# Optimization experiments

Measured on AMD Instinct MI355X. Metric: run time of the kernel, lower is better.

Reference implementation:

```python
import jax, jax.numpy as jnp
import numpy as np

DIM = 768
H = 12  # num_heads -> head width W = 64 (required by internal reshapes)


def setup_inputs() -> dict:
    key = jax.random.key(0)
    ks = jax.random.split(key, 16)
    B, S = 1, 128  # V = Q = A = 128 tokens
    d = {
        "v": jax.random.normal(ks[0], (B, S, DIM), jnp.float32),
        "q": jax.random.normal(ks[1], (B, S, DIM), jnp.float32),
        "a": jax.random.normal(ks[2], (B, S, DIM), jnp.float32),
        "v_mask": jnp.ones((B, S), jnp.bool_),  # unused by the module, kept for signature parity
        "q_mask": jnp.ones((B, S), jnp.bool_),
        "a_mask": jnp.ones((B, S), jnp.bool_),
    }
    scale = 0.02
    names = ["Wv", "Wq", "Wa", "Wvo", "Wqo", "Wao"]
    for i, n in enumerate(names):
        d[n] = jax.random.normal(ks[3 + i], (DIM, DIM), jnp.float32) * scale
        d["b" + n[1:].lower()] = jnp.zeros((DIM,), jnp.float32)
    return d


def _heads(x):
    # (B, S, D) -> (B, H, S, W)
    B, S, D = x.shape
    return x.reshape(B, S, H, D // H).transpose(0, 2, 1, 3)


def reference(v, q, a, v_mask, q_mask, a_mask,
              Wv, bv, Wq, bq, Wa, ba, Wvo, bvo, Wqo, bqo, Wao, bao):
    B, Sv, D = v.shape
    Sq, Sa = q.shape[1], a.shape[1]
    W = D // H
    nv, nq, na = Sv // 8, Sq // 8, Sa // 8

    # first projections (masks are unused in the original forward)
    vp = v @ Wv + bv
    qp = q @ Wq + bq
    ap = a @ Wa + ba
    # output projections are applied to the ALREADY-projected tensors (as in source)
    vo = vp @ Wvo + bvo
    qo = qp @ Wqo + bqo
    ao = ap @ Wao + bao

    vh, qh, ah = _heads(vp), _heads(qp), _heads(ap)          # (B,H,S,W)
    voh, qoh, aoh = _heads(vo), _heads(qo), _heads(ao)

    # trilinear scores: (B,H,V,Q,A)
    att = jnp.einsum('bhvw,bhqw,bhaw->bhvqa', vh, qh, ah) / jnp.sqrt(jnp.asarray(W, vh.dtype))
    K = nv * nq * na
    # faithful to source: view(-1, H, nv*nq*na) then softmax over last axis, view back
    att = jax.nn.softmax(att.reshape(-1, H, K), axis=-1)
    att = att.reshape(-1, H, nv, nq, na)  # dropout p=0 -> identity
    B2 = att.shape[0]

    # source uses att.size(2) (= nv) for ALL three reshapes (requires V=Q=A)
    vor = voh.reshape(B2, H, nv, -1)
    qor = qoh.reshape(B2, H, nv, -1)
    aor = aoh.reshape(B2, H, nv, -1)

    v_out = jnp.einsum('bhvqa,bhvw->bvhw', att, vor).reshape(-1, DIM)
    q_out = jnp.einsum('bhvqa,bhqw->bqhw', att, qor).reshape(-1, DIM)
    a_out = jnp.einsum('bhvqa,bhaw->bahw', att, aor).reshape(-1, DIM)
    return (v_out, q_out, a_out)
```

## Files before the change

kernel.cpp:

```cpp
#include <hip/hip_runtime.h>


#define DIM   768
#define SEQ   128
#define NH    12
#define HW    64
#define PROJ_ELEMS (SEQ * DIM)
#define WELEMS     (DIM * DIM)
#define QOUT_OFF   98304
#define AOUT_OFF   196608

typedef _Float16 f16x8 __attribute__((ext_vector_type(8)));
typedef float    f32x4 __attribute__((ext_vector_type(4)));

__device__ __forceinline__ float exp2_fast(float x) {
    float r;
    asm("v_exp_f32 %0, %1\n\ts_nop 1" : "=v"(r) : "v"(x));
    return r;
}
#define LOG2E_DIV8 0.18033688011112042f

__global__ __launch_bounds__(256) void prep_w_kernel(
    const float* __restrict__ W0, const float* __restrict__ W1, const float* __restrict__ W2,
    const float* __restrict__ W3, const float* __restrict__ W4, const float* __restrict__ W5,
    _Float16* __restrict__ Wt)
{
    const int z = blockIdx.z;
    const float* W = (z == 0) ? W0 : (z == 1) ? W1 : (z == 2) ? W2
                   : (z == 3) ? W3 : (z == 4) ? W4 : W5;
    _Float16* WtM = Wt + z * WELEMS;
    __shared__ _Float16 T[64][72];
    const int t  = threadIdx.x;
    const int k0 = blockIdx.x * 64;
    const int n0 = blockIdx.y * 64;
    const int c4 = (t & 15) * 4;
    #pragma unroll
    for (int p = 0; p < 4; ++p) {
        const int r = (t >> 4) + 16 * p;
        f32x4 wv = *(const f32x4*)&W[(k0 + r) * DIM + n0 + c4];
        T[c4 + 0][r] = (_Float16)wv[0];
        T[c4 + 1][r] = (_Float16)wv[1];
        T[c4 + 2][r] = (_Float16)wv[2];
        T[c4 + 3][r] = (_Float16)wv[3];
    }
    __syncthreads();
    const int c2 = (t & 7) * 8;
    #pragma unroll
    for (int p = 0; p < 2; ++p) {
        const int r = (t >> 3) + 32 * p;
        *(f16x8*)&WtM[(n0 + r) * DIM + k0 + c2] = *(const f16x8*)&T[r][c2];
    }
}

__global__ __launch_bounds__(64) void proj_kernel(
    const void* __restrict__ A0, const void* __restrict__ A1, const void* __restrict__ A2,
    const _Float16* __restrict__ T0, const _Float16* __restrict__ T1, const _Float16* __restrict__ T2,
    const float* __restrict__ b0, const float* __restrict__ b1, const float* __restrict__ b2,
    void* __restrict__ C0, void* __restrict__ C1, void* __restrict__ C2,
    int in_f32, int out_f16)
{
    const int mat = blockIdx.z;
    const void* __restrict__ A     = (mat == 0) ? A0 : (mat == 1) ? A1 : A2;
    const _Float16* __restrict__ T = (mat == 0) ? T0 : (mat == 1) ? T1 : T2;
    const float* __restrict__ bb   = (mat == 0) ? b0 : (mat == 1) ? b1 : b2;
    void* __restrict__ C           = (mat == 0) ? C0 : (mat == 1) ? C1 : C2;

    const int m0   = blockIdx.x * 16;
    const int n0   = blockIdx.y * 16;
    const int lane = threadIdx.x & 63;
    const int fm   = lane & 15;
    const int fk   = (lane >> 4) << 3;

    const _Float16* pb = T + (n0 + fm) * DIM + fk;
    f32x4 acc = (f32x4){0.f, 0.f, 0.f, 0.f};

    if (in_f32) {
        const float* pa = (const float*)A + (m0 + fm) * DIM + fk;
        #pragma unroll 4
        for (int s = 0; s < 24; ++s) {
            const f32x4 lo = *(const f32x4*)(pa + 32 * s);
            const f32x4 hi = *(const f32x4*)(pa + 32 * s + 4);
            f16x8 af;
            af[0] = (_Float16)lo[0]; af[1] = (_Float16)lo[1];
            af[2] = (_Float16)lo[2]; af[3] = (_Float16)lo[3];
            af[4] = (_Float16)hi[0]; af[5] = (_Float16)hi[1];
            af[6] = (_Float16)hi[2]; af[7] = (_Float16)hi[3];
            const f16x8 wf = *(const f16x8*)(pb + 32 * s);
            acc = __builtin_amdgcn_mfma_f32_16x16x32_f16(af, wf, acc, 0, 0, 0);
        }
    } else {
        const _Float16* pa = (const _Float16*)A + (m0 + fm) * DIM + fk;
        #pragma unroll 4
        for (int s = 0; s < 24; ++s) {
            const f16x8 af = *(const f16x8*)(pa + 32 * s);
            const f16x8 wf = *(const f16x8*)(pb + 32 * s);
            acc = __builtin_amdgcn_mfma_f32_16x16x32_f16(af, wf, acc, 0, 0, 0);
        }
    }

    const int col  = n0 + fm;
    const int row0 = m0 + ((lane >> 4) << 2);
    const float bi = bb[col];
    #pragma unroll
    for (int rr = 0; rr < 4; ++rr) {
        const float val = acc[rr] + bi;
        if (out_f16) ((_Float16*)C)[(row0 + rr) * DIM + col] = (_Float16)val;
        else         ((float*)C)[(row0 + rr) * DIM + col]    = val;
    }
}

__global__ __launch_bounds__(256) void fused_attn_kernel(
    const _Float16* __restrict__ vpH, const _Float16* __restrict__ qpH,
    const _Float16* __restrict__ apH,
    const float* __restrict__ vo, const float* __restrict__ qo, const float* __restrict__ ao,
    float* __restrict__ out)
{
    const int vtok = blockIdx.x;
    const int h    = blockIdx.y;

    __shared__ _Float16 vqL[128][72];
    __shared__ _Float16 ahL[128][72];

    const int t    = threadIdx.x;
    const int w    = t >> 6;
    const int lane = t & 63;
    const int fm   = lane & 15;
    const int fk   = (lane >> 4) << 3;

    {
        const int r  = t >> 1;
        const int kh = (t & 1) << 5;
        const _Float16* pq = qpH + r    * DIM + h * HW + kh;
        const _Float16* pv = vpH + vtok * DIM + h * HW + kh;
        const _Float16* pa = apH + r    * DIM + h * HW + kh;
        #pragma unroll
        for (int u = 0; u < 4; ++u) {
            const f16x8 qv = *(const f16x8*)(pq + 8 * u);
            const f16x8 vv = *(const f16x8*)(pv + 8 * u);
            *(f16x8*)&vqL[r][kh + 8 * u] = qv * vv;
            *(f16x8*)&ahL[r][kh + 8 * u] = *(const f16x8*)(pa + 8 * u);
        }
    }
    __syncthreads();

    f32x4 acc[2][8];
    #pragma unroll
    for (int qt = 0; qt < 2; ++qt)
        #pragma unroll
        for (int at = 0; at < 8; ++at)
            acc[qt][at] = (f32x4){0.f, 0.f, 0.f, 0.f};

    const int q0 = 32 * w;
    #pragma unroll
    for (int ks = 0; ks < 2; ++ks) {
        const f16x8 af0 = *(const f16x8*)&vqL[q0 + fm     ][32 * ks + fk];
        const f16x8 af1 = *(const f16x8*)&vqL[q0 + 16 + fm][32 * ks + fk];
        #pragma unroll
        for (int at = 0; at < 8; ++at) {
            const f16x8 bf = *(const f16x8*)&ahL[16 * at + fm][32 * ks + fk];
            acc[0][at] = __builtin_amdgcn_mfma_f32_16x16x32_f16(af0, bf, acc[0][at], 0, 0, 0);
            acc[1][at] = __builtin_amdgcn_mfma_f32_16x16x32_f16(af1, bf, acc[1][at], 0, 0, 0);
        }
    }

    float sv[2][2] = {{0.f, 0.f}, {0.f, 0.f}};
    float sq[2][8];
    #pragma unroll
    for (int i = 0; i < 2; ++i)
        #pragma unroll
        for (int j = 0; j < 8; ++j) sq[i][j] = 0.f;
    float sa = 0.f;
    #pragma unroll
    for (int qt = 0; qt < 2; ++qt)
        #pragma unroll
        for (int at = 0; at < 8; ++at)
            #pragma unroll
            for (int rr = 0; rr < 4; ++rr) {
                const float e = exp2_fast(acc[qt][at][rr] * LOG2E_DIV8);
                sv[qt][rr >> 1] += e;
                sq[rr & 1][at]  += e;
                sa += e;
            }

    sa += __shfl_xor(sa, 16);
    sa += __shfl_xor(sa, 32);
    float tot = sa;
    tot += __shfl_xor(tot, 1);
    tot += __shfl_xor(tot, 2);
    tot += __shfl_xor(tot, 4);
    tot += __shfl_xor(tot, 8);
    const bool b0 = lane & 1;
    const bool b1 = lane & 2;
    float sF;
    {
        float snd0 = b0 ? sv[0][0] : sv[1][0];
        float snd1 = b0 ? sv[0][1] : sv[1][1];
        float r0 = __shfl_xor(snd0, 1);
        float r1 = __shfl_xor(snd1, 1);
        float s0 = (b0 ? sv[1][0] : sv[0][0]) + r0;
        float s1 = (b0 ? sv[1][1] : sv[0][1]) + r1;
        float snd = b1 ? s0 : s1;
        float r2 = __shfl_xor(snd, 2);
        sF = (b1 ? s1 : s0) + r2;
    }
    sF += __shfl_xor(sF, 4);
    sF += __shfl_xor(sF, 8);
    float s[16];
    #pragma unroll
    for (int i = 0; i < 2; ++i)
        #pragma unroll
        for (int j = 0; j < 8; ++j) s[i * 8 + j] = sq[i][j];
    #pragma unroll
    for (int k = 0; k < 4; ++k) {
        const int d = 1 << k;
        const int m = 16 >> (k + 1);
        const bool b = (lane >> k) & 1;
        #pragma unroll
        for (int x = 0; x < m; ++x) {
            const float snd = b ? s[x] : s[x + m];
            const float rcv = __shfl_xor(snd, d);
            s[x] = (b ? s[x + m] : s[x]) + rcv;
        }
    }
    s[0] += __shfl_xor(s[0], 16);
    s[0] += __shfl_xor(s[0], 32);

    const int g  = h * 512 + vtok * 4 + w;
    const int b2 = g / 12;
    const int h2 = g - b2 * 12;
    const float invZ = 1.0f / tot;
    const int obase = vtok * DIM + h * HW + w * 16;

    if (fm < 4) {
        const int quad = lane >> 4;
        const int bin  = (fm & 1) * 8 + quad * 2 + ((fm >> 1) & 1);
        out[(b2 * 16 + bin) * 12 + h2] = sF * invZ * vo[obase + bin];
    }
    if (lane < 16) {
        const int qbin = 8 * (lane & 1) + 4 * ((lane >> 1) & 1)
                       + 2 * ((lane >> 2) & 1) + (lane >> 3);
        out[QOUT_OFF + (b2 * 16 + qbin) * 12 + h2] = s[0] * invZ * qo[obase + qbin];
        out[AOUT_OFF + (b2 * 16 + lane) * 12 + h2] = sa   * invZ * ao[obase + lane];
    }
}

extern "C" void kernel_launch(void* const* d_in, const int* in_sizes, int n_in,
                              void* d_out, int out_size, void* d_ws, size_t ws_size,
                              hipStream_t stream)
{
    const float* v   = (const float*)d_in[0];
    const float* q   = (const float*)d_in[1];
    const float* a   = (const float*)d_in[2];
    const float* Wv  = (const float*)d_in[6];
    const float* bv  = (const float*)d_in[7];
    const float* Wq  = (const float*)d_in[8];
    const float* bq  = (const float*)d_in[9];
    const float* Wa  = (const float*)d_in[10];
    const float* ba  = (const float*)d_in[11];
    const float* Wvo = (const float*)d_in[12];
    const float* bvo = (const float*)d_in[13];
    const float* Wqo = (const float*)d_in[14];
    const float* bqo = (const float*)d_in[15];
    const float* Wao = (const float*)d_in[16];
    const float* bao = (const float*)d_in[17];

    float* out = (float*)d_out;

    _Float16* Wt  = (_Float16*)d_ws;
    _Float16* vpH = Wt + 6 * WELEMS;
    _Float16* qpH = vpH + PROJ_ELEMS;
    _Float16* apH = qpH + PROJ_ELEMS;
    float*    vo  = (float*)(apH + PROJ_ELEMS);
    float*    qo  = vo + PROJ_ELEMS;
    float*    ao  = qo + PROJ_ELEMS;

    prep_w_kernel<<<dim3(12, 12, 6), 256, 0, stream>>>(
        Wv, Wq, Wa, Wvo, Wqo, Wao, Wt);
    proj_kernel<<<dim3(8, 48, 3), 64, 0, stream>>>(
        v, q, a, Wt, Wt + WELEMS, Wt + 2 * WELEMS,
        bv, bq, ba, vpH, qpH, apH, 1, 1);
    proj_kernel<<<dim3(8, 48, 3), 64, 0, stream>>>(
        vpH, qpH, apH, Wt + 3 * WELEMS, Wt + 4 * WELEMS, Wt + 5 * WELEMS,
        bvo, bqo, bao, vo, qo, ao, 0, 0);
    fused_attn_kernel<<<dim3(SEQ, NH), 256, 0, stream>>>(
        vpH, qpH, apH, vo, qo, ao, out);
}
```

Baseline: 144.0 us.

## Merge all stages into one cooperative persistent kernel with grid syncs

Replaces the four separate launches (weight transpose, two projection GEMMs, attention) with a single cooperative kernel of 512 blocks that moves between stages via grid-wide syncs. In the attention stage each block now handles three consecutive (head, token) pairs and reuses the staged Q/A head tiles in shared memory across them. The v*q product is formed in registers instead of in shared memory. The aim is to remove launch gaps and repeated head-tile loads, at the cost of grid-sync overhead and lower parallelism per stage.

```diff
diff --git a/kernel.cpp b/kernel.cpp
--- a/kernel.cpp
+++ b/kernel.cpp
@@ -1,4 +1,7 @@
 #include <hip/hip_runtime.h>
+#include <hip/hip_cooperative_groups.h>
+
+namespace cg = cooperative_groups;
 
 
 #define DIM   768
@@ -20,227 +23,250 @@
 }
 #define LOG2E_DIV8 0.18033688011112042f
 
-__global__ __launch_bounds__(256) void prep_w_kernel(
-    const float* __restrict__ W0, const float* __restrict__ W1, const float* __restrict__ W2,
-    const float* __restrict__ W3, const float* __restrict__ W4, const float* __restrict__ W5,
-    _Float16* __restrict__ Wt)
-{
-    const int z = blockIdx.z;
-    const float* W = (z == 0) ? W0 : (z == 1) ? W1 : (z == 2) ? W2
-                   : (z == 3) ? W3 : (z == 4) ? W4 : W5;
-    _Float16* WtM = Wt + z * WELEMS;
-    __shared__ _Float16 T[64][72];
-    const int t  = threadIdx.x;
-    const int k0 = blockIdx.x * 64;
-    const int n0 = blockIdx.y * 64;
-    const int c4 = (t & 15) * 4;
-    #pragma unroll
-    for (int p = 0; p < 4; ++p) {
-        const int r = (t >> 4) + 16 * p;
-        f32x4 wv = *(const f32x4*)&W[(k0 + r) * DIM + n0 + c4];
-        T[c4 + 0][r] = (_Float16)wv[0];
-        T[c4 + 1][r] = (_Float16)wv[1];
-        T[c4 + 2][r] = (_Float16)wv[2];
-        T[c4 + 3][r] = (_Float16)wv[3];
-    }
-    __syncthreads();
-    const int c2 = (t & 7) * 8;
-    #pragma unroll
-    for (int p = 0; p < 2; ++p) {
-        const int r = (t >> 3) + 32 * p;
-        *(f16x8*)&WtM[(n0 + r) * DIM + k0 + c2] = *(const f16x8*)&T[r][c2];
-    }
-}
-
-__global__ __launch_bounds__(64) void proj_kernel(
-    const void* __restrict__ A0, const void* __restrict__ A1, const void* __restrict__ A2,
-    const _Float16* __restrict__ T0, const _Float16* __restrict__ T1, const _Float16* __restrict__ T2,
-    const float* __restrict__ b0, const float* __restrict__ b1, const float* __restrict__ b2,
-    void* __restrict__ C0, void* __restrict__ C1, void* __restrict__ C2,
-    int in_f32, int out_f16)
-{
-    const int mat = blockIdx.z;
-    const void* __restrict__ A     = (mat == 0) ? A0 : (mat == 1) ? A1 : A2;
-    const _Float16* __restrict__ T = (mat == 0) ? T0 : (mat == 1) ? T1 : T2;
-    const float* __restrict__ bb   = (mat == 0) ? b0 : (mat == 1) ? b1 : b2;
-    void* __restrict__ C           = (mat == 0) ? C0 : (mat == 1) ? C1 : C2;
-
-    const int m0   = blockIdx.x * 16;
-    const int n0   = blockIdx.y * 16;
-    const int lane = threadIdx.x & 63;
-    const int fm   = lane & 15;
-    const int fk   = (lane >> 4) << 3;
-
-    const _Float16* pb = T + (n0 + fm) * DIM + fk;
-    f32x4 acc = (f32x4){0.f, 0.f, 0.f, 0.f};
-
-    if (in_f32) {
-        const float* pa = (const float*)A + (m0 + fm) * DIM + fk;
-        #pragma unroll 4
-        for (int s = 0; s < 24; ++s) {
-            const f32x4 lo = *(const f32x4*)(pa + 32 * s);
-            const f32x4 hi = *(const f32x4*)(pa + 32 * s + 4);
-            f16x8 af;
-            af[0] = (_Float16)lo[0]; af[1] = (_Float16)lo[1];
-            af[2] = (_Float16)lo[2]; af[3] = (_Float16)lo[3];
-            af[4] = (_Float16)hi[0]; af[5] = (_Float16)hi[1];
-            af[6] = (_Float16)hi[2]; af[7] = (_Float16)hi[3];
-            const f16x8 wf = *(const f16x8*)(pb + 32 * s);
-            acc = __builtin_amdgcn_mfma_f32_16x16x32_f16(af, wf, acc, 0, 0, 0);
-        }
-    } else {
-        const _Float16* pa = (const _Float16*)A + (m0 + fm) * DIM + fk;
-        #pragma unroll 4
-        for (int s = 0; s < 24; ++s) {
-            const f16x8 af = *(const f16x8*)(pa + 32 * s);
-            const f16x8 wf = *(const f16x8*)(pb + 32 * s);
-            acc = __builtin_amdgcn_mfma_f32_16x16x32_f16(af, wf, acc, 0, 0, 0);
-        }
-    }
-
-    const int col  = n0 + fm;
-    const int row0 = m0 + ((lane >> 4) << 2);
-    const float bi = bb[col];
-    #pragma unroll
-    for (int rr = 0; rr < 4; ++rr) {
-        const float val = acc[rr] + bi;
-        if (out_f16) ((_Float16*)C)[(row0 + rr) * DIM + col] = (_Float16)val;
-        else         ((float*)C)[(row0 + rr) * DIM + col]    = val;
-    }
-}
-
-__global__ __launch_bounds__(256) void fused_attn_kernel(
-    const _Float16* __restrict__ vpH, const _Float16* __restrict__ qpH,
-    const _Float16* __restrict__ apH,
-    const float* __restrict__ vo, const float* __restrict__ qo, const float* __restrict__ ao,
+__global__ __launch_bounds__(256, 4) void mono_kernel(
+    const float* __restrict__ v, const float* __restrict__ q, const float* __restrict__ a,
+    const float* __restrict__ Wv, const float* __restrict__ bv,
+    const float* __restrict__ Wq, const float* __restrict__ bq,
+    const float* __restrict__ Wa, const float* __restrict__ ba,
+    const float* __restrict__ Wvo, const float* __restrict__ bvo,
+    const float* __restrict__ Wqo, const float* __restrict__ bqo,
+    const float* __restrict__ Wao, const float* __restrict__ bao,
+    _Float16* __restrict__ Wt,
+    _Float16* __restrict__ vpH, _Float16* __restrict__ qpH, _Float16* __restrict__ apH,
+    float* __restrict__ vo, float* __restrict__ qo, float* __restrict__ ao,
     float* __restrict__ out)
 {
-    const int vtok = blockIdx.x;
-    const int h    = blockIdx.y;
-
-    __shared__ _Float16 vqL[128][72];
-    __shared__ _Float16 ahL[128][72];
-
+    cg::grid_group grid = cg::this_grid();
+    const int bid  = blockIdx.x;
     const int t    = threadIdx.x;
     const int w    = t >> 6;
     const int lane = t & 63;
     const int fm   = lane & 15;
     const int fk   = (lane >> 4) << 3;
 
+    __shared__ _Float16 shQ[128][72];
+    __shared__ _Float16 shA[128][72];
+
+    for (int tile = bid; tile < 864; tile += 512) {
+        const int z  = tile / 144;
+        const int r2 = tile - z * 144;
+        const int k0 = (r2 / 12) * 64;
+        const int n0 = (r2 - (r2 / 12) * 12) * 64;
+        const float* W = (z == 0) ? Wv : (z == 1) ? Wq : (z == 2) ? Wa
+                       : (z == 3) ? Wvo : (z == 4) ? Wqo : Wao;
+        _Float16* WtM = Wt + z * WELEMS;
+        __syncthreads();
+        const int c4 = (t & 15) * 4;
+        #pragma unroll
+        for (int p = 0; p < 4; ++p) {
+            const int r = (t >> 4) + 16 * p;
+            f32x4 wv = *(const f32x4*)&W[(k0 + r) * DIM + n0 + c4];
+            shQ[c4 + 0][r] = (_Float16)wv[0];
+            shQ[c4 + 1][r] = (_Float16)wv[1];
+            shQ[c4 + 2][r] = (_Float16)wv[2];
+            shQ[c4 + 3][r] = (_Float16)wv[3];
+        }
+        __syncthreads();
+        const int c2 = (t & 7) * 8;
+        #pragma unroll
+        for (int p = 0; p < 2; ++p) {
+            const int r = (t >> 3) + 32 * p;
+            *(f16x8*)&WtM[(n0 + r) * DIM + k0 + c2] = *(const f16x8*)&shQ[r][c2];
+        }
+    }
+    grid.sync();
+
     {
-        const int r  = t >> 1;
-        const int kh = (t & 1) << 5;
-        const _Float16* pq = qpH + r    * DIM + h * HW + kh;
-        const _Float16* pv = vpH + vtok * DIM + h * HW + kh;
-        const _Float16* pa = apH + r    * DIM + h * HW + kh;
-        #pragma unroll
-        for (int u = 0; u < 4; ++u) {
-            const f16x8 qv = *(const f16x8*)(pq + 8 * u);
-            const f16x8 vv = *(const f16x8*)(pv + 8 * u);
-            *(f16x8*)&vqL[r][kh + 8 * u] = qv * vv;
-            *(f16x8*)&ahL[r][kh + 8 * u] = *(const f16x8*)(pa + 8 * u);
+        const int gw = bid * 4 + w;
+        if (gw < 1152) {
+            const int mat = gw / 384;
+            const int rem = gw - mat * 384;
+            const int m0 = (rem / 48) * 16;
+            const int n0 = (rem - (rem / 48) * 48) * 16;
+            const float* A      = (mat == 0) ? v : (mat == 1) ? q : a;
+            const _Float16* T   = Wt + mat * WELEMS;
+            const float* bb     = (mat == 0) ? bv : (mat == 1) ? bq : ba;
+            _Float16* C         = (mat == 0) ? vpH : (mat == 1) ? qpH : apH;
+            const float* pa     = A + (m0 + fm) * DIM + fk;
+            const _Float16* pb  = T + (n0 + fm) * DIM + fk;
+            f32x4 acc = (f32x4){0.f, 0.f, 0.f, 0.f};
+            #pragma unroll 4
+            for (int s = 0; s < 24; ++s) {
+                const f32x4 lo = *(const f32x4*)(pa + 32 * s);
+                const f32x4 hi = *(const f32x4*)(pa + 32 * s + 4);
+                f16x8 af;
+                af[0] = (_Float16)lo[0]; af[1] = (_Float16)lo[1];
+                af[2] = (_Float16)lo[2]; af[3] = (_Float16)lo[3];
+                af[4] = (_Float16)hi[0]; af[5] = (_Float16)hi[1];
+                af[6] = (_Float16)hi[2]; af[7] = (_Float16)hi[3];
+                const f16x8 wf = *(const f16x8*)(pb + 32 * s);
+                acc = __builtin_amdgcn_mfma_f32_16x16x32_f16(af, wf, acc, 0, 0, 0);
+            }
+            const int col  = n0 + fm;
+            const int row0 = m0 + ((lane >> 4) << 2);
+            const float bi = bb[col];
+            #pragma unroll
+            for (int rr = 0; rr < 4; ++rr)
+                C[(row0 + rr) * DIM + col] = (_Float16)(acc[rr] + bi);
         }
     }
-    __syncthreads();
-
-    f32x4 acc[2][8];
-    #pragma unroll
-    for (int qt = 0; qt < 2; ++qt)
-        #pragma unroll
-        for (int at = 0; at < 8; ++at)
-            acc[qt][at] = (f32x4){0.f, 0.f, 0.f, 0.f};
-
-    const int q0 = 32 * w;
-    #pragma unroll
-    for (int ks = 0; ks < 2; ++ks) {
-        const f16x8 af0 = *(const f16x8*)&vqL[q0 + fm     ][32 * ks + fk];
-        const f16x8 af1 = *(const f16x8*)&vqL[q0 + 16 + fm][32 * ks + fk];
-        #pragma unroll
-        for (int at = 0; at < 8; ++at) {
-            const f16x8 bf = *(const f16x8*)&ahL[16 * at + fm][32 * ks + fk];
-            acc[0][at] = __builtin_amdgcn_mfma_f32_16x16x32_f16(af0, bf, acc[0][at], 0, 0, 0);
-            acc[1][at] = __builtin_amdgcn_mfma_f32_16x16x32_f16(af1, bf, acc[1][at], 0, 0, 0);
+    grid.sync();
+
+    {
+        const int gw = bid * 4 + w;
+        if (gw < 1152) {
+            const int mat = gw / 384;
+            const int rem = gw - mat * 384;
+            const int m0 = (rem / 48) * 16;
+            const int n0 = (rem - (rem / 48) * 48) * 16;
+            const _Float16* A  = (mat == 0) ? vpH : (mat == 1) ? qpH : apH;
+            const _Float16* T  = Wt + (3 + mat) * WELEMS;
+            const float* bb    = (mat == 0) ? bvo : (mat == 1) ? bqo : bao;
+            float* C           = (mat == 0) ? vo : (mat == 1) ? qo : ao;
+            const _Float16* pa = A + (m0 + fm) * DIM + fk;
+            const _Float16* pb = T + (n0 + fm) * DIM + fk;
+            f32x4 acc = (f32x4){0.f, 0.f, 0.f, 0.f};
+            #pragma unroll 4
+            for (int s = 0; s < 24; ++s) {
+                const f16x8 af = *(const f16x8*)(pa + 32 * s);
+                const f16x8 wf = *(const f16x8*)(pb + 32 * s);
+                acc = __builtin_amdgcn_mfma_f32_16x16x32_f16(af, wf, acc, 0, 0, 0);
+            }
+            const int col  = n0 + fm;
+            const int row0 = m0 + ((lane >> 4) << 2);
+            const float bi = bb[col];
+            #pragma unroll
+            for (int rr = 0; rr < 4; ++rr)
+                C[(row0 + rr) * DIM + col] = acc[rr] + bi;
         }
     }
-
-    float sv[2][2] = {{0.f, 0.f}, {0.f, 0.f}};
-    float sq[2][8];
-    #pragma unroll
-    for (int i = 0; i < 2; ++i)
-        #pragma unroll
-        for (int j = 0; j < 8; ++j) sq[i][j] = 0.f;
-    float sa = 0.f;
-    #pragma unroll
-    for (int qt = 0; qt < 2; ++qt)
-        #pragma unroll
-        for (int at = 0; at < 8; ++at)
-            #pragma unroll
-            for (int rr = 0; rr < 4; ++rr) {
-                const float e = exp2_fast(acc[qt][at][rr] * LOG2E_DIV8);
-                sv[qt][rr >> 1] += e;
-                sq[rr & 1][at]  += e;
-                sa += e;
-            }
-
-    sa += __shfl_xor(sa, 16);
-    sa += __shfl_xor(sa, 32);
-    float tot = sa;
-    tot += __shfl_xor(tot, 1);
-    tot += __shfl_xor(tot, 2);
-    tot += __shfl_xor(tot, 4);
-    tot += __shfl_xor(tot, 8);
+    grid.sync();
+
+    int cur_h = -1;
     const bool b0 = lane & 1;
     const bool b1 = lane & 2;
-    float sF;
-    {
-        float snd0 = b0 ? sv[0][0] : sv[1][0];
-        float snd1 = b0 ? sv[0][1] : sv[1][1];
-        float r0 = __shfl_xor(snd0, 1);
-        float r1 = __shfl_xor(snd1, 1);
-        float s0 = (b0 ? sv[1][0] : sv[0][0]) + r0;
-        float s1 = (b0 ? sv[1][1] : sv[0][1]) + r1;
-        float snd = b1 ? s0 : s1;
-        float r2 = __shfl_xor(snd, 2);
-        sF = (b1 ? s1 : s0) + r2;
-    }
-    sF += __shfl_xor(sF, 4);
-    sF += __shfl_xor(sF, 8);
-    float s[16];
-    #pragma unroll
-    for (int i = 0; i < 2; ++i)
-        #pragma unroll
-        for (int j = 0; j < 8; ++j) s[i * 8 + j] = sq[i][j];
-    #pragma unroll
-    for (int k = 0; k < 4; ++k) {
-        const int d = 1 << k;
-        const int m = 16 >> (k + 1);
-        const bool b = (lane >> k) & 1;
-        #pragma unroll
-        for (int x = 0; x < m; ++x) {
-            const float snd = b ? s[x] : s[x + m];
-            const float rcv = __shfl_xor(snd, d);
-            s[x] = (b ? s[x + m] : s[x]) + rcv;
-        }
-    }
-    s[0] += __shfl_xor(s[0], 16);
-    s[0] += __shfl_xor(s[0], 32);
-
-    const int g  = h * 512 + vtok * 4 + w;
-    const int b2 = g / 12;
-    const int h2 = g - b2 * 12;
-    const float invZ = 1.0f / tot;
-    const int obase = vtok * DIM + h * HW + w * 16;
-
-    if (fm < 4) {
-        const int quad = lane >> 4;
-        const int bin  = (fm & 1) * 8 + quad * 2 + ((fm >> 1) & 1);
-        out[(b2 * 16 + bin) * 12 + h2] = sF * invZ * vo[obase + bin];
-    }
-    if (lane < 16) {
-        const int qbin = 8 * (lane & 1) + 4 * ((lane >> 1) & 1)
-                       + 2 * ((lane >> 2) & 1) + (lane >> 3);
-        out[QOUT_OFF + (b2 * 16 + qbin) * 12 + h2] = s[0] * invZ * qo[obase + qbin];
-        out[AOUT_OFF + (b2 * 16 + lane) * 12 + h2] = sa   * invZ * ao[obase + lane];
+    for (int i = 0; i < 3; ++i) {
+        const int p    = 3 * bid + i;
+        const int h    = p >> 7;
+        const int vtok = p & 127;
+
+        if (h != cur_h) {
+            __syncthreads();
+            const int r  = t >> 1;
+            const int kh = (t & 1) << 5;
+            const _Float16* pq = qpH + r * DIM + h * HW + kh;
+            const _Float16* pa = apH + r * DIM + h * HW + kh;
+            #pragma unroll
+            for (int u = 0; u < 4; ++u) {
+                *(f16x8*)&shQ[r][kh + 8 * u] = *(const f16x8*)(pq + 8 * u);
+                *(f16x8*)&shA[r][kh + 8 * u] = *(const f16x8*)(pa + 8 * u);
+            }
+            __syncthreads();
+            cur_h = h;
+        }
+
+        f16x8 vf[2];
+        #pragma unroll
+        for (int ks = 0; ks < 2; ++ks)
+            vf[ks] = *(const f16x8*)&vpH[vtok * DIM + h * HW + 32 * ks + fk];
+
+        f32x4 acc[2][8];
+        #pragma unroll
+        for (int qt = 0; qt < 2; ++qt)
+            #pragma unroll
+            for (int at = 0; at < 8; ++at)
+                acc[qt][at] = (f32x4){0.f, 0.f, 0.f, 0.f};
+
+        const int q0 = 32 * w;
+        #pragma unroll
+        for (int ks = 0; ks < 2; ++ks) {
+            const f16x8 af0 = (*(const f16x8*)&shQ[q0 + fm     ][32 * ks + fk]) * vf[ks];
+            const f16x8 af1 = (*(const f16x8*)&shQ[q0 + 16 + fm][32 * ks + fk]) * vf[ks];
+            #pragma unroll
+            for (int at = 0; at < 8; ++at) {
+                const f16x8 bf = *(const f16x8*)&shA[16 * at + fm][32 * ks + fk];
+                acc[0][at] = __builtin_amdgcn_mfma_f32_16x16x32_f16(af0, bf, acc[0][at], 0, 0, 0);
+                acc[1][at] = __builtin_amdgcn_mfma_f32_16x16x32_f16(af1, bf, acc[1][at], 0, 0, 0);
+            }
+        }
+
+        float sv[2][2] = {{0.f, 0.f}, {0.f, 0.f}};
+        float sq[2][8];
+        #pragma unroll
+        for (int ii = 0; ii < 2; ++ii)
+            #pragma unroll
+            for (int j = 0; j < 8; ++j) sq[ii][j] = 0.f;
+        float sa = 0.f;
+        #pragma unroll
+        for (int qt = 0; qt < 2; ++qt)
+            #pragma unroll
+            for (int at = 0; at < 8; ++at)
+                #pragma unroll
+                for (int rr = 0; rr < 4; ++rr) {
+                    const float e = exp2_fast(acc[qt][at][rr] * LOG2E_DIV8);
+                    sv[qt][rr >> 1] += e;
+                    sq[rr & 1][at]  += e;
+                    sa += e;
+                }
+
+        sa += __shfl_xor(sa, 16);
+        sa += __shfl_xor(sa, 32);
+        float tot = sa;
+        tot += __shfl_xor(tot, 1);
+        tot += __shfl_xor(tot, 2);
+        tot += __shfl_xor(tot, 4);
+        tot += __shfl_xor(tot, 8);
+        float sF;
+        {
+            float snd0 = b0 ? sv[0][0] : sv[1][0];
+            float snd1 = b0 ? sv[0][1] : sv[1][1];
+            float r0 = __shfl_xor(snd0, 1);
+            float r1 = __shfl_xor(snd1, 1);
+            float s0 = (b0 ? sv[1][0] : sv[0][0]) + r0;
+            float s1 = (b0 ? sv[1][1] : sv[0][1]) + r1;
+            float snd = b1 ? s0 : s1;
+            float r2 = __shfl_xor(snd, 2);
+            sF = (b1 ? s1 : s0) + r2;
+        }
+        sF += __shfl_xor(sF, 4);
+        sF += __shfl_xor(sF, 8);
+        float s[16];
+        #pragma unroll
+        for (int ii = 0; ii < 2; ++ii)
+            #pragma unroll
+            for (int j = 0; j < 8; ++j) s[ii * 8 + j] = sq[ii][j];
+        #pragma unroll
+        for (int k = 0; k < 4; ++k) {
+            const int d = 1 << k;
+            const int m = 16 >> (k + 1);
+            const bool b = (lane >> k) & 1;
+            #pragma unroll
+            for (int x = 0; x < m; ++x) {
+                const float snd = b ? s[x] : s[x + m];
+                const float rcv = __shfl_xor(snd, d);
+                s[x] = (b ? s[x + m] : s[x]) + rcv;
+            }
+        }
+        s[0] += __shfl_xor(s[0], 16);
+        s[0] += __shfl_xor(s[0], 32);
+
+        const int g  = h * 512 + vtok * 4 + w;
+        const int b2 = g / 12;
+        const int h2 = g - b2 * 12;
+        const float invZ = 1.0f / tot;
+        const int obase = vtok * DIM + h * HW + w * 16;
+
+        if (fm < 4) {
+            const int quad = lane >> 4;
+            const int bin  = (fm & 1) * 8 + quad * 2 + ((fm >> 1) & 1);
+            out[(b2 * 16 + bin) * 12 + h2] = sF * invZ * vo[obase + bin];
+        }
+        if (lane < 16) {
+            const int qbin = 8 * (lane & 1) + 4 * ((lane >> 1) & 1)
+                           + 2 * ((lane >> 2) & 1) + (lane >> 3);
+            out[QOUT_OFF + (b2 * 16 + qbin) * 12 + h2] = s[0] * invZ * qo[obase + qbin];
+            out[AOUT_OFF + (b2 * 16 + lane) * 12 + h2] = sa   * invZ * ao[obase + lane];
+        }
     }
 }
 
@@ -274,14 +300,14 @@
     float*    qo  = vo + PROJ_ELEMS;
     float*    ao  = qo + PROJ_ELEMS;
 
-    prep_w_kernel<<<dim3(12, 12, 6), 256, 0, stream>>>(
-        Wv, Wq, Wa, Wvo, Wqo, Wao, Wt);
-    proj_kernel<<<dim3(8, 48, 3), 64, 0, stream>>>(
-        v, q, a, Wt, Wt + WELEMS, Wt + 2 * WELEMS,
-        bv, bq, ba, vpH, qpH, apH, 1, 1);
-    proj_kernel<<<dim3(8, 48, 3), 64, 0, stream>>>(
-        vpH, qpH, apH, Wt + 3 * WELEMS, Wt + 4 * WELEMS, Wt + 5 * WELEMS,
-        bvo, bqo, bao, vo, qo, ao, 0, 0);
-    fused_attn_kernel<<<dim3(SEQ, NH), 256, 0, stream>>>(
-        vpH, qpH, apH, vo, qo, ao, out);
+    void* args[] = {
+        (void*)&v, (void*)&q, (void*)&a,
+        (void*)&Wv, (void*)&bv, (void*)&Wq, (void*)&bq,
+        (void*)&Wa, (void*)&ba, (void*)&Wvo, (void*)&bvo,
+        (void*)&Wqo, (void*)&bqo, (void*)&Wao, (void*)&bao,
+        (void*)&Wt, (void*)&vpH, (void*)&qpH, (void*)&apH,
+        (void*)&vo, (void*)&qo, (void*)&ao, (void*)&out
+    };
+    hipLaunchCooperativeKernel((const void*)mono_kernel,
+                               dim3(512), dim3(256), args, 0, stream);
 }
```

Result: slower. 340.5 us (+136.4%).

## Fuse projections into two kernels and compute output projections inside attention

Applied to the files above, without the earlier changes.

Merges four launches into two. The first kernel does the first projections straight from fp32 weights staged transposed in shared memory, and in the same grid transposes the output-projection weights to fp16. The attention kernel now computes the 192 output-projection values it needs for its token and head with dot2 instructions, so the separate vo/qo/ao GEMM and its fp32 intermediates go away. This cuts launch overhead and intermediate traffic, but each attention block recomputes a 3x64x768 dot product per (token, head), and output projections now accumulate from fp16 inputs.

```diff
diff --git a/kernel.cpp b/kernel.cpp
--- a/kernel.cpp
+++ b/kernel.cpp
@@ -11,6 +11,7 @@
 #define AOUT_OFF   196608
 
 typedef _Float16 f16x8 __attribute__((ext_vector_type(8)));
+typedef _Float16 f16x2 __attribute__((ext_vector_type(2)));
 typedef float    f32x4 __attribute__((ext_vector_type(4)));
 
 __device__ __forceinline__ float exp2_fast(float x) {
@@ -20,99 +21,121 @@
 }
 #define LOG2E_DIV8 0.18033688011112042f
 
-__global__ __launch_bounds__(256) void prep_w_kernel(
-    const float* __restrict__ W0, const float* __restrict__ W1, const float* __restrict__ W2,
-    const float* __restrict__ W3, const float* __restrict__ W4, const float* __restrict__ W5,
-    _Float16* __restrict__ Wt)
+__device__ __forceinline__ float dot2acc(f16x2 a, f16x2 b, float c) {
+#if __has_builtin(__builtin_amdgcn_fdot2)
+    return __builtin_amdgcn_fdot2(a, b, c, false);
+#else
+    return fmaf((float)a[0], (float)b[0], fmaf((float)a[1], (float)b[1], c));
+#endif
+}
+
+__global__ __launch_bounds__(256) void k1_kernel(
+    const float* __restrict__ v, const float* __restrict__ q, const float* __restrict__ a,
+    const float* __restrict__ Wv, const float* __restrict__ bv,
+    const float* __restrict__ Wq, const float* __restrict__ bq,
+    const float* __restrict__ Wa, const float* __restrict__ ba,
+    const float* __restrict__ Wvo, const float* __restrict__ Wqo, const float* __restrict__ Wao,
+    _Float16* __restrict__ Wt2,
+    _Float16* __restrict__ vpH, _Float16* __restrict__ qpH, _Float16* __restrict__ apH)
 {
-    const int z = blockIdx.z;
-    const float* W = (z == 0) ? W0 : (z == 1) ? W1 : (z == 2) ? W2
-                   : (z == 3) ? W3 : (z == 4) ? W4 : W5;
-    _Float16* WtM = Wt + z * WELEMS;
+    __shared__ _Float16 Wl[16][776];
     __shared__ _Float16 T[64][72];
-    const int t  = threadIdx.x;
-    const int k0 = blockIdx.x * 64;
-    const int n0 = blockIdx.y * 64;
-    const int c4 = (t & 15) * 4;
-    #pragma unroll
-    for (int p = 0; p < 4; ++p) {
-        const int r = (t >> 4) + 16 * p;
-        f32x4 wv = *(const f32x4*)&W[(k0 + r) * DIM + n0 + c4];
-        T[c4 + 0][r] = (_Float16)wv[0];
-        T[c4 + 1][r] = (_Float16)wv[1];
-        T[c4 + 2][r] = (_Float16)wv[2];
-        T[c4 + 3][r] = (_Float16)wv[3];
-    }
-    __syncthreads();
-    const int c2 = (t & 7) * 8;
-    #pragma unroll
-    for (int p = 0; p < 2; ++p) {
-        const int r = (t >> 3) + 32 * p;
-        *(f16x8*)&WtM[(n0 + r) * DIM + k0 + c2] = *(const f16x8*)&T[r][c2];
-    }
-}
-
-__global__ __launch_bounds__(64) void proj_kernel(
-    const void* __restrict__ A0, const void* __restrict__ A1, const void* __restrict__ A2,
-    const _Float16* __restrict__ T0, const _Float16* __restrict__ T1, const _Float16* __restrict__ T2,
-    const float* __restrict__ b0, const float* __restrict__ b1, const float* __restrict__ b2,
-    void* __restrict__ C0, void* __restrict__ C1, void* __restrict__ C2,
-    int in_f32, int out_f16)
-{
-    const int mat = blockIdx.z;
-    const void* __restrict__ A     = (mat == 0) ? A0 : (mat == 1) ? A1 : A2;
-    const _Float16* __restrict__ T = (mat == 0) ? T0 : (mat == 1) ? T1 : T2;
-    const float* __restrict__ bb   = (mat == 0) ? b0 : (mat == 1) ? b1 : b2;
-    void* __restrict__ C           = (mat == 0) ? C0 : (mat == 1) ? C1 : C2;
-
-    const int m0   = blockIdx.x * 16;
-    const int n0   = blockIdx.y * 16;
-    const int lane = threadIdx.x & 63;
-    const int fm   = lane & 15;
-    const int fk   = (lane >> 4) << 3;
-
-    const _Float16* pb = T + (n0 + fm) * DIM + fk;
-    f32x4 acc = (f32x4){0.f, 0.f, 0.f, 0.f};
-
-    if (in_f32) {
-        const float* pa = (const float*)A + (m0 + fm) * DIM + fk;
+
+    const int bid = blockIdx.x;
+    const int t   = threadIdx.x;
+
+    if (bid < 144) {
+        const int mat = bid / 48;
+        const int n0  = (bid - mat * 48) * 16;
+        const float* __restrict__ A  = (mat == 0) ? v : (mat == 1) ? q : a;
+        const float* __restrict__ W  = (mat == 0) ? Wv : (mat == 1) ? Wq : Wa;
+        const float* __restrict__ bb = (mat == 0) ? bv : (mat == 1) ? bq : ba;
+        _Float16* __restrict__ C     = (mat == 0) ? vpH : (mat == 1) ? qpH : apH;
+
+        #pragma unroll
+        for (int p = 0; p < 3; ++p) {
+            const int kk = t + 256 * p;
+            #pragma unroll
+            for (int c = 0; c < 4; ++c) {
+                const f32x4 wv4 = *(const f32x4*)&W[kk * DIM + n0 + 4 * c];
+                Wl[4 * c + 0][kk] = (_Float16)wv4[0];
+                Wl[4 * c + 1][kk] = (_Float16)wv4[1];
+                Wl[4 * c + 2][kk] = (_Float16)wv4[2];
+                Wl[4 * c + 3][kk] = (_Float16)wv4[3];
+            }
+        }
+        __syncthreads();
+
+        const int w    = t >> 6;
+        const int lane = t & 63;
+        const int fm   = lane & 15;
+        const int fk   = (lane >> 4) << 3;
+        const float* pa0 = A + (32 * w + fm) * DIM + fk;
+        const float* pa1 = pa0 + 16 * DIM;
+
+        f32x4 acc0 = (f32x4){0.f, 0.f, 0.f, 0.f};
+        f32x4 acc1 = (f32x4){0.f, 0.f, 0.f, 0.f};
         #pragma unroll 4
         for (int s = 0; s < 24; ++s) {
-            const f32x4 lo = *(const f32x4*)(pa + 32 * s);
-            const f32x4 hi = *(const f32x4*)(pa + 32 * s + 4);
-            f16x8 af;
-            af[0] = (_Float16)lo[0]; af[1] = (_Float16)lo[1];
-            af[2] = (_Float16)lo[2]; af[3] = (_Float16)lo[3];
-            af[4] = (_Float16)hi[0]; af[5] = (_Float16)hi[1];
-            af[6] = (_Float16)hi[2]; af[7] = (_Float16)hi[3];
-            const f16x8 wf = *(const f16x8*)(pb + 32 * s);
-            acc = __builtin_amdgcn_mfma_f32_16x16x32_f16(af, wf, acc, 0, 0, 0);
+            const f32x4 l0 = *(const f32x4*)(pa0 + 32 * s);
+            const f32x4 h0 = *(const f32x4*)(pa0 + 32 * s + 4);
+            const f32x4 l1 = *(const f32x4*)(pa1 + 32 * s);
+            const f32x4 h1 = *(const f32x4*)(pa1 + 32 * s + 4);
+            f16x8 a0, a1;
+            a0[0] = (_Float16)l0[0]; a0[1] = (_Float16)l0[1];
+            a0[2] = (_Float16)l0[2]; a0[3] = (_Float16)l0[3];
+            a0[4] = (_Float16)h0[0]; a0[5] = (_Float16)h0[1];
+            a0[6] = (_Float16)h0[2]; a0[7] = (_Float16)h0[3];
+            a1[0] = (_Float16)l1[0]; a1[1] = (_Float16)l1[1];
+            a1[2] = (_Float16)l1[2]; a1[3] = (_Float16)l1[3];
+            a1[4] = (_Float16)h1[0]; a1[5] = (_Float16)h1[1];
+            a1[6] = (_Float16)h1[2]; a1[7] = (_Float16)h1[3];
+            const f16x8 bf = *(const f16x8*)&Wl[fm][32 * s + fk];
+            acc0 = __builtin_amdgcn_mfma_f32_16x16x32_f16(a0, bf, acc0, 0, 0, 0);
+            acc1 = __builtin_amdgcn_mfma_f32_16x16x32_f16(a1, bf, acc1, 0, 0, 0);
+        }
+
+        const int col   = n0 + fm;
+        const int quad4 = (lane >> 4) << 2;
+        const float bi  = bb[col];
+        #pragma unroll
+        for (int rr = 0; rr < 4; ++rr) {
+            C[(32 * w + quad4 + rr) * DIM + col]      = (_Float16)(acc0[rr] + bi);
+            C[(32 * w + 16 + quad4 + rr) * DIM + col] = (_Float16)(acc1[rr] + bi);
         }
     } else {
-        const _Float16* pa = (const _Float16*)A + (m0 + fm) * DIM + fk;
-        #pragma unroll 4
-        for (int s = 0; s < 24; ++s) {
-            const f16x8 af = *(const f16x8*)(pa + 32 * s);
-            const f16x8 wf = *(const f16x8*)(pb + 32 * s);
-            acc = __builtin_amdgcn_mfma_f32_16x16x32_f16(af, wf, acc, 0, 0, 0);
-        }
-    }
-
-    const int col  = n0 + fm;
-    const int row0 = m0 + ((lane >> 4) << 2);
-    const float bi = bb[col];
-    #pragma unroll
-    for (int rr = 0; rr < 4; ++rr) {
-        const float val = acc[rr] + bi;
-        if (out_f16) ((_Float16*)C)[(row0 + rr) * DIM + col] = (_Float16)val;
-        else         ((float*)C)[(row0 + rr) * DIM + col]    = val;
-    }
-}
-
-__global__ __launch_bounds__(256) void fused_attn_kernel(
+        const int tt = bid - 144;
+        const int z  = tt / 144;
+        const int r2 = tt - z * 144;
+        const int k0 = (r2 / 12) * 64;
+        const int n0 = (r2 - (r2 / 12) * 12) * 64;
+        const float* W = (z == 0) ? Wvo : (z == 1) ? Wqo : Wao;
+        _Float16* WtM  = Wt2 + z * WELEMS;
+        const int c4 = (t & 15) * 4;
+        #pragma unroll
+        for (int p = 0; p < 4; ++p) {
+            const int r = (t >> 4) + 16 * p;
+            const f32x4 wv4 = *(const f32x4*)&W[(k0 + r) * DIM + n0 + c4];
+            T[c4 + 0][r] = (_Float16)wv4[0];
+            T[c4 + 1][r] = (_Float16)wv4[1];
+            T[c4 + 2][r] = (_Float16)wv4[2];
+            T[c4 + 3][r] = (_Float16)wv4[3];
+        }
+        __syncthreads();
+        const int c2 = (t & 7) * 8;
+        #pragma unroll
+        for (int p = 0; p < 2; ++p) {
+            const int r = (t >> 3) + 32 * p;
+            *(f16x8*)&WtM[(n0 + r) * DIM + k0 + c2] = *(const f16x8*)&T[r][c2];
+        }
+    }
+}
+
+__global__ __launch_bounds__(256) void k2_kernel(
     const _Float16* __restrict__ vpH, const _Float16* __restrict__ qpH,
     const _Float16* __restrict__ apH,
-    const float* __restrict__ vo, const float* __restrict__ qo, const float* __restrict__ ao,
+    const _Float16* __restrict__ Wt2,
+    const float* __restrict__ bvo, const float* __restrict__ bqo, const float* __restrict__ bao,
     float* __restrict__ out)
 {
     const int vtok = blockIdx.x;
@@ -120,6 +143,8 @@
 
     __shared__ _Float16 vqL[128][72];
     __shared__ _Float16 ahL[128][72];
+    __shared__ _Float16 rowBuf[3 * DIM];
+    __shared__ float    oBuf[192];
 
     const int t    = threadIdx.x;
     const int w    = t >> 6;
@@ -141,7 +166,37 @@
             *(f16x8*)&ahL[r][kh + 8 * u] = *(const f16x8*)(pa + 8 * u);
         }
     }
+    for (int c = t; c < 288; c += 256) {
+        const int mat = c / 96;
+        const int k0  = (c - mat * 96) * 8;
+        const _Float16* src = ((mat == 0) ? vpH : (mat == 1) ? qpH : apH) + vtok * DIM + k0;
+        *(f16x8*)&rowBuf[mat * DIM + k0] = *(const f16x8*)src;
+    }
     __syncthreads();
+
+    float dotv = 0.f;
+    if (t < 192) {
+        const int mat = t >> 6;
+        const int n   = t & 63;
+        const _Float16* wrow = Wt2 + mat * WELEMS + (h * HW + n) * DIM;
+        const _Float16* rrow = &rowBuf[mat * DIM];
+        float d0 = 0.f, d1 = 0.f, d2 = 0.f, d3 = 0.f;
+        #pragma unroll 4
+        for (int k8 = 0; k8 < 96; ++k8) {
+            const f16x8 rv = *(const f16x8*)&rrow[8 * k8];
+            const f16x8 wv = *(const f16x8*)&wrow[8 * k8];
+            d0 = dot2acc(__builtin_shufflevector(rv, rv, 0, 1),
+                         __builtin_shufflevector(wv, wv, 0, 1), d0);
+            d1 = dot2acc(__builtin_shufflevector(rv, rv, 2, 3),
+                         __builtin_shufflevector(wv, wv, 2, 3), d1);
+            d2 = dot2acc(__builtin_shufflevector(rv, rv, 4, 5),
+                         __builtin_shufflevector(wv, wv, 4, 5), d2);
+            d3 = dot2acc(__builtin_shufflevector(rv, rv, 6, 7),
+                         __builtin_shufflevector(wv, wv, 6, 7), d3);
+        }
+        const float* bb = (mat == 0) ? bvo : (mat == 1) ? bqo : bao;
+        dotv = (d0 + d1) + (d2 + d3) + bb[h * HW + n];
+    }
 
     f32x4 acc[2][8];
     #pragma unroll
@@ -225,22 +280,24 @@
     s[0] += __shfl_xor(s[0], 16);
     s[0] += __shfl_xor(s[0], 32);
 
+    if (t < 192) oBuf[t] = dotv;
+    __syncthreads();
+
     const int g  = h * 512 + vtok * 4 + w;
     const int b2 = g / 12;
     const int h2 = g - b2 * 12;
     const float invZ = 1.0f / tot;
-    const int obase = vtok * DIM + h * HW + w * 16;
 
     if (fm < 4) {
         const int quad = lane >> 4;
         const int bin  = (fm & 1) * 8 + quad * 2 + ((fm >> 1) & 1);
-        out[(b2 * 16 + bin) * 12 + h2] = sF * invZ * vo[obase + bin];
+        out[(b2 * 16 + bin) * 12 + h2] = sF * invZ * oBuf[w * 16 + bin];
     }
     if (lane < 16) {
         const int qbin = 8 * (lane & 1) + 4 * ((lane >> 1) & 1)
                        + 2 * ((lane >> 2) & 1) + (lane >> 3);
-        out[QOUT_OFF + (b2 * 16 + qbin) * 12 + h2] = s[0] * invZ * qo[obase + qbin];
-        out[AOUT_OFF + (b2 * 16 + lane) * 12 + h2] = sa   * invZ * ao[obase + lane];
+        out[QOUT_OFF + (b2 * 16 + qbin) * 12 + h2] = s[0] * invZ * oBuf[64 + w * 16 + qbin];
+        out[AOUT_OFF + (b2 * 16 + lane) * 12 + h2] = sa   * invZ * oBuf[128 + w * 16 + lane];
     }
 }
 
@@ -266,22 +323,14 @@
 
     float* out = (float*)d_out;
 
-    _Float16* Wt  = (_Float16*)d_ws;
-    _Float16* vpH = Wt + 6 * WELEMS;
+    _Float16* Wt2 = (_Float16*)d_ws;
+    _Float16* vpH = Wt2 + 3 * WELEMS;
     _Float16* qpH = vpH + PROJ_ELEMS;
     _Float16* apH = qpH + PROJ_ELEMS;
-    float*    vo  = (float*)(apH + PROJ_ELEMS);
-    float*    qo  = vo + PROJ_ELEMS;
-    float*    ao  = qo + PROJ_ELEMS;
-
-    prep_w_kernel<<<dim3(12, 12, 6), 256, 0, stream>>>(
-        Wv, Wq, Wa, Wvo, Wqo, Wao, Wt);
-    proj_kernel<<<dim3(8, 48, 3), 64, 0, stream>>>(
-        v, q, a, Wt, Wt + WELEMS, Wt + 2 * WELEMS,
-        bv, bq, ba, vpH, qpH, apH, 1, 1);
-    proj_kernel<<<dim3(8, 48, 3), 64, 0, stream>>>(
-        vpH, qpH, apH, Wt + 3 * WELEMS, Wt + 4 * WELEMS, Wt + 5 * WELEMS,
-        bvo, bqo, bao, vo, qo, ao, 0, 0);
-    fused_attn_kernel<<<dim3(SEQ, NH), 256, 0, stream>>>(
-        vpH, qpH, apH, vo, qo, ao, out);
-}
+
+    k1_kernel<<<dim3(576), 256, 0, stream>>>(
+        v, q, a, Wv, bv, Wq, bq, Wa, ba, Wvo, Wqo, Wao,
+        Wt2, vpH, qpH, apH);
+    k2_kernel<<<dim3(SEQ, NH), 256, 0, stream>>>(
+        vpH, qpH, apH, Wt2, bvo, bqo, bao, out);
+}
```

After: 173.4 us. 20.4% more time.
